# Performance work log

Measured on AMD Instinct MI355X. Metric: run time of the kernel, lower is better.

The kernel has to match this reference:

```python
import jax, jax.numpy as jnp
import numpy as np

DIM = 768
HEADS = 6
LEVELS = 3
POINTS = 4
HID = int(DIM * 0.25)  # 192
B = 4
H0 = 64
W0 = 64
NQ = H0 * W0
SHAPES = [(128, 128), (64, 64), (32, 32)]
NV = sum(h * w for h, w in SHAPES)
EPS = 1e-6


def _ln(x, g, b):
    m = x.mean(-1, keepdims=True)
    v = ((x - m) ** 2).mean(-1, keepdims=True)
    return (x - m) / jnp.sqrt(v + EPS) * g + b


def _bilinear(img, grid, Hl, Wl):
    # img: [BH, Hl*Wl, d], grid: [BH, Np, 2] in [-1,1] (x=width, y=height)
    # grid_sample semantics: bilinear, padding zeros, align_corners=False
    gx, gy = grid[..., 0], grid[..., 1]
    x = (gx + 1) * (Wl * 0.5) - 0.5
    y = (gy + 1) * (Hl * 0.5) - 0.5
    x0 = jnp.floor(x)
    y0 = jnp.floor(y)
    wx = x - x0
    wy = y - y0
    x0i = x0.astype(jnp.int32)
    y0i = y0.astype(jnp.int32)

    def corner(xi, yi, wgt):
        valid = (xi >= 0) & (xi < Wl) & (yi >= 0) & (yi < Hl)
        idx = jnp.clip(yi, 0, Hl - 1) * Wl + jnp.clip(xi, 0, Wl - 1)
        v = jnp.take_along_axis(img, idx[..., None], axis=1)
        return v * (wgt * valid)[..., None]

    return (corner(x0i, y0i, (1 - wx) * (1 - wy))
            + corner(x0i + 1, y0i, wx * (1 - wy))
            + corner(x0i, y0i + 1, (1 - wx) * wy)
            + corner(x0i + 1, y0i + 1, wx * wy))


def setup_inputs() -> dict:
    key = jax.random.key(0)
    ks = jax.random.split(key, 24)
    s = 0.02
    inp = {
        'query': jax.random.normal(ks[0], (B, NQ, DIM), jnp.float32),
        'reference_points': jax.random.uniform(ks[1], (B, NQ, LEVELS, 2), jnp.float32),
        'feat': jax.random.normal(ks[2], (B, NV, DIM), jnp.float32),
        'spatial_shapes': jnp.array(SHAPES, dtype=jnp.int32),
        'level_start_index': jnp.array(np.cumsum([0] + [h * w for h, w in SHAPES])[:-1], dtype=jnp.int32),
        'H': H0,
        'W': W0,
        'qn_g': jnp.ones((DIM,)), 'qn_b': jnp.zeros((DIM,)),
        'fn_g': jnp.ones((DIM,)), 'fn_b': jnp.zeros((DIM,)),
        'off_w': jax.random.normal(ks[3], (DIM, HEADS * LEVELS * POINTS * 2)) * s,
        'off_b': jax.random.normal(ks[4], (HEADS * LEVELS * POINTS * 2,)) * s,
        'aw_w': jax.random.normal(ks[5], (DIM, HEADS * LEVELS * POINTS)) * s,
        'aw_b': jnp.zeros((HEADS * LEVELS * POINTS,)),
        'vp_w': jax.random.normal(ks[6], (DIM, DIM)) * s,
        'vp_b': jnp.zeros((DIM,)),
        'op_w': jax.random.normal(ks[7], (DIM, DIM)) * s,
        'op_b': jnp.zeros((DIM,)),
        'ffn_g': jnp.ones((DIM,)), 'ffn_b': jnp.zeros((DIM,)),
        'fc1_w': jax.random.normal(ks[8], (DIM, HID)) * s,
        'fc1_b': jnp.zeros((HID,)),
        'dw_w': jax.random.normal(ks[9], (3, 3, 1, HID)) * s,
        'dw_b': jnp.zeros((HID,)),
        'fc2_w': jax.random.normal(ks[10], (HID, DIM)) * s,
        'fc2_b': jnp.zeros((DIM,)),
    }
    return inp


def reference(query, reference_points, feat, spatial_shapes, level_start_index, H, W,
              qn_g, qn_b, fn_g, fn_b, off_w, off_b, aw_w, aw_b, vp_w, vp_b, op_w, op_b,
              ffn_g, ffn_b, fc1_w, fc1_b, dw_w, dw_b, fc2_w, fc2_b):
    shapes = [(int(h), int(w)) for h, w in np.asarray(spatial_shapes)]
    starts = np.cumsum([0] + [h * w for h, w in shapes])[:-1]
    Bq, Nq, C = query.shape
    d = C // HEADS

    q = _ln(query, qn_g, qn_b)                       # query_norm
    v = _ln(feat, fn_g, fn_b) @ vp_w + vp_b          # feat_norm + value_proj
    v = v.reshape(Bq, -1, HEADS, d)

    off = (q @ off_w + off_b).reshape(Bq, Nq, HEADS, LEVELS, POINTS, 2)
    aw = (q @ aw_w + aw_b).reshape(Bq, Nq, HEADS, LEVELS * POINTS)
    aw = jax.nn.softmax(aw, axis=-1).reshape(Bq, Nq, HEADS, LEVELS, POINTS)

    # offset normalizer is (W, H) per level
    norm = jnp.array([[w_, h_] for h_, w_ in shapes], dtype=query.dtype)
    loc = reference_points[:, :, None, :, None, :] + off / norm[None, None, None, :, None, :]
    grids = 2.0 * loc - 1.0                          # [B,Nq,heads,L,P,2]

    outs = []
    for l, (hl, wl) in enumerate(shapes):
        vl = v[:, starts[l]:starts[l] + hl * wl]     # [B, hl*wl, heads, d]
        vl = vl.transpose(0, 2, 1, 3).reshape(Bq * HEADS, hl * wl, d)
        g = grids[:, :, :, l].transpose(0, 2, 1, 3, 4).reshape(Bq * HEADS, Nq * POINTS, 2)
        s = _bilinear(vl, g, hl, wl).reshape(Bq, HEADS, Nq, POINTS, d)
        outs.append(s)
    samp = jnp.stack(outs, axis=3)                   # [B,heads,Nq,L,P,d]
    w_att = aw.transpose(0, 2, 1, 3, 4)              # [B,heads,Nq,L,P]
    out = (samp * w_att[..., None]).sum(axis=(3, 4)) # [B,heads,Nq,d]
    out = out.transpose(0, 2, 1, 3).reshape(Bq, Nq, C)
    attn = out @ op_w + op_b + q                     # mmcv adds identity (=normed query)

    x = query + attn

    # ConvFFN: fc1 -> DWConv -> GELU -> fc2, residual
    y = _ln(x, ffn_g, ffn_b) @ fc1_w + fc1_b         # [B,Nq,HID]
    y2 = y.reshape(Bq, H, W, HID)
    y2 = jax.lax.conv_general_dilated(
        y2, dw_w, window_strides=(1, 1), padding='SAME',
        feature_group_count=HID,
        dimension_numbers=('NHWC', 'HWIO', 'NHWC')) + dw_b
    y = jax.nn.gelu(y2.reshape(Bq, Nq, HID), approximate=False)
    y = y @ fc2_w + fc2_b
    return x + y
```

## Files before the change

### kernel.cpp

```cpp
#include <hip/hip_runtime.h>
#include <hip/hip_bf16.h>

constexpr int kDIM = 768;
constexpr int kHEADS = 6;
constexpr int kLEVELS = 3;
constexpr int kPOINTS = 4;
constexpr int kHID = 192;
constexpr int kB = 4;
constexpr int kH0 = 64;
constexpr int kW0 = 64;
constexpr int kNQ = kH0 * kW0;
constexpr int kNV = 21504;
constexpr int kDH = 128;
constexpr float kEPS = 1e-6f;
constexpr int kOAW = 256;

typedef __attribute__((ext_vector_type(8))) short short8;
typedef __attribute__((ext_vector_type(4))) float floatx4;
typedef __attribute__((ext_vector_type(4))) unsigned int uintx4;

__device__ __forceinline__ float bf2f(__hip_bfloat16 x) { return __bfloat162float(x); }
__device__ __forceinline__ float bfu2f(unsigned short u) { return __uint_as_float(((unsigned)u) << 16); }
__device__ __forceinline__ unsigned short f2bfu(float f) {
  __hip_bfloat16 h = __float2bfloat16(f);
  return *reinterpret_cast<unsigned short*>(&h);
}

__global__ __launch_bounds__(256) void ln_bf16_kernel(
    const float* __restrict__ x, const float* __restrict__ g,
    const float* __restrict__ b, __hip_bfloat16* __restrict__ out)
{
  constexpr int MT = 8;
  int tid = threadIdx.x, grp = tid >> 5, lane = tid & 31;
  size_t row = (size_t)blockIdx.x * MT + grp;
  const float* xr = x + row * kDIM;
  float buf[kDIM / 32];
  float s = 0.f;
#pragma unroll
  for (int i = 0; i < kDIM / 32; ++i) { float v = xr[lane + i * 32]; buf[i] = v; s += v; }
  for (int d = 16; d > 0; d >>= 1) s += __shfl_down(s, d, 32);
  float mean = __shfl(s, 0, 32) * (1.f / kDIM);
  float vs = 0.f;
#pragma unroll
  for (int i = 0; i < kDIM / 32; ++i) { float d = buf[i] - mean; vs += d * d; }
  for (int d = 16; d > 0; d >>= 1) vs += __shfl_down(vs, d, 32);
  float rstd = rsqrtf(__shfl(vs, 0, 32) * (1.f / kDIM) + kEPS);
  __hip_bfloat16* orow = out + row * kDIM;
#pragma unroll
  for (int i = 0; i < kDIM / 32; ++i) {
    int k = lane + i * 32;
    orow[k] = __float2bfloat16((buf[i] - mean) * rstd * g[k] + b[k]);
  }
}

__global__ __launch_bounds__(256) void transpose_w_kernel(
    const float* __restrict__ w, __hip_bfloat16* __restrict__ wt)
{
  int t = blockIdx.x * 256 + threadIdx.x;
  int n = t / kDIM, k = t % kDIM;
  wt[t] = __float2bfloat16(w[(size_t)k * kDIM + n]);
}

template <int K, int N, int NPAD>
__global__ __launch_bounds__(256) void prep_wt_kernel(
    const float* __restrict__ w, const float* __restrict__ b,
    __hip_bfloat16* __restrict__ wt, float* __restrict__ bp)
{
  int t = blockIdx.x * 256 + threadIdx.x;
  int n = t / K, k = t % K;
  float v = (n < N) ? w[(size_t)k * N + n] : 0.f;
  wt[t] = __float2bfloat16(v);
  if (bp != nullptr && t < NPAD) bp[t] = (t < N) ? b[t] : 0.f;
}

__global__ __launch_bounds__(256) void prep_offaw_w_kernel(
    const float* __restrict__ ow, const float* __restrict__ aww,
    const float* __restrict__ ob, const float* __restrict__ awb,
    __hip_bfloat16* __restrict__ wt, float* __restrict__ bias)
{
  int t = blockIdx.x * 256 + threadIdx.x;
  int n = t / kDIM, k = t % kDIM;
  float v = 0.f;
  if (n < 144)       v = ow[(size_t)k * 144 + n];
  else if (n < 216)  v = aww[(size_t)k * 72 + (n - 144)];
  wt[t] = __float2bfloat16(v);
  if (t < kOAW) {
    float b = 0.f;
    if (t < 144)       b = ob[t];
    else if (t < 216)  b = awb[t - 144];
    bias[t] = b;
  }
}

template <int EPI, int KK>
__global__ __launch_bounds__(256) void gemm_bt_kernel(
    const unsigned short* __restrict__ A, const unsigned short* __restrict__ Bt,
    const float* __restrict__ bias,
    __hip_bfloat16* __restrict__ outB,
    const __hip_bfloat16* __restrict__ qln, const float* __restrict__ query,
    float* __restrict__ outF)
{
  constexpr int K = KK;
  constexpr int LDC = (EPI == 2) ? kOAW : kDIM;
  __shared__ unsigned short sA[128 * 64];
  __shared__ unsigned short sB[128 * 64];
  int tid = threadIdx.x;
  int wave = tid >> 6, lane = tid & 63;
  int tm = blockIdx.x * 128, tn = blockIdx.y * 128;
  int wm = (wave & 1) * 64, wn = (wave >> 1) * 64;
  floatx4 acc[4][4] = {};

  for (int k0 = 0; k0 < K; k0 += 64) {
    __syncthreads();
#pragma unroll
    for (int i = 0; i < 4; ++i) {
      int id = i * 256 + tid;
      int m = id >> 3, c = id & 7;
      uintx4 va = *(const uintx4*)(A + (size_t)(tm + m) * K + k0 + c * 8);
      *(uintx4*)((char*)sA + m * 128 + ((c ^ (m & 7)) * 16)) = va;
      uintx4 vb = *(const uintx4*)(Bt + (size_t)(tn + m) * K + k0 + c * 8);
      *(uintx4*)((char*)sB + m * 128 + ((c ^ (m & 7)) * 16)) = vb;
    }
    __syncthreads();
#pragma unroll
    for (int s = 0; s < 2; ++s) {
      int kc = s * 4 + (lane >> 4);
      short8 af[4], bfr[4];
#pragma unroll
      for (int i = 0; i < 4; ++i) {
        int mm = wm + i * 16 + (lane & 15);
        af[i] = *(const short8*)((const char*)sA + mm * 128 + ((kc ^ (mm & 7)) * 16));
        int nn = wn + i * 16 + (lane & 15);
        bfr[i] = *(const short8*)((const char*)sB + nn * 128 + ((kc ^ (nn & 7)) * 16));
      }
#pragma unroll
      for (int i = 0; i < 4; ++i)
#pragma unroll
        for (int j = 0; j < 4; ++j)
          acc[i][j] = __builtin_amdgcn_mfma_f32_16x16x32_bf16(af[i], bfr[j], acc[i][j], 0, 0, 0);
    }
  }

  int r0 = (lane >> 4) * 4, cc = lane & 15;
#pragma unroll
  for (int i = 0; i < 4; ++i) {
    int rowb = tm + wm + i * 16 + r0;
#pragma unroll
    for (int j = 0; j < 4; ++j) {
      int col = tn + wn + j * 16 + cc;
      float bv = bias[col];
#pragma unroll
      for (int r = 0; r < 4; ++r) {
        size_t o = (size_t)(rowb + r) * LDC + col;
        float val = acc[i][j][r] + bv;
        if constexpr (EPI == 0) {
          outB[o] = __float2bfloat16(val);
        } else if constexpr (EPI == 1) {
          outF[o] = val + bf2f(qln[o]) + query[o];
        } else if constexpr (EPI == 2) {
          outF[o] = val;
        } else {
          outF[o] = val + query[o];
        }
      }
    }
  }
}

__global__ __launch_bounds__(256) void aw_softmax_kernel(float* __restrict__ raw)
{
  int t = blockIdx.x * 256 + threadIdx.x;
  int row = t / kHEADS, h = t % kHEADS;
  float* p = raw + (size_t)row * kOAW + 144 + h * 12;
  float v[12];
  float m = -1e30f;
#pragma unroll
  for (int j = 0; j < 12; ++j) { v[j] = p[j]; m = fmaxf(m, v[j]); }
  float den = 0.f;
#pragma unroll
  for (int j = 0; j < 12; ++j) { v[j] = expf(v[j] - m); den += v[j]; }
  float inv = 1.f / den;
#pragma unroll
  for (int j = 0; j < 12; ++j) p[j] = v[j] * inv;
}

__global__ __launch_bounds__(192) void sample_kernel(
    const float* __restrict__ offaw,
    const float* __restrict__ refp, const __hip_bfloat16* __restrict__ v,
    __hip_bfloat16* __restrict__ samp)
{
  __shared__ int   idx_s[72][4];
  __shared__ float w_s[72][4];
  int bq = blockIdx.x;
  int b = bq >> 12;
  int tid = threadIdx.x;

  if (tid < 72) {
    const int LH[3] = {128, 64, 32};
    const int LST[3] = {0, 16384, 20480};
    int h2 = tid / 12, j = tid % 12, l = j >> 2, p = j & 3;
    int Wl = LH[l];
    const float* base = offaw + (size_t)bq * kOAW;
    float rx = refp[(size_t)bq * 6 + l * 2 + 0];
    float ry = refp[(size_t)bq * 6 + l * 2 + 1];
    float ox = base[h2 * 24 + l * 8 + p * 2 + 0];
    float oy = base[h2 * 24 + l * 8 + p * 2 + 1];
    float wgt = base[144 + h2 * 12 + l * 4 + p];
    float xx = rx * Wl + ox - 0.5f;
    float yy = ry * Wl + oy - 0.5f;
    float x0f = floorf(xx), y0f = floorf(yy);
    int x0 = (int)x0f, y0 = (int)y0f;
    float wx = xx - x0f, wy = yy - y0f;
#pragma unroll
    for (int cy = 0; cy < 2; ++cy) {
#pragma unroll
      for (int cx = 0; cx < 2; ++cx) {
        int xi = x0 + cx, yi = y0 + cy;
        bool valid = (xi >= 0) && (xi < Wl) && (yi >= 0) && (yi < Wl);
        int xc = min(max(xi, 0), Wl - 1), yc = min(max(yi, 0), Wl - 1);
        float cw = (cx ? wx : 1.f - wx) * (cy ? wy : 1.f - wy);
        idx_s[tid][cy * 2 + cx] = (LST[l] + yc * Wl + xc) * kDIM;
        w_s[tid][cy * 2 + cx] = valid ? cw * wgt : 0.f;
      }
    }
  }
  __syncthreads();

  int h = tid >> 5, c0 = (tid & 31) * 4;
  const __hip_bfloat16* vb = v + (size_t)b * kNV * kDIM + h * kDH + c0;
  float a0 = 0.f, a1 = 0.f, a2 = 0.f, a3 = 0.f;
#pragma unroll
  for (int j = 0; j < 12; ++j) {
    int t = h * 12 + j;
    int4 ii = *(const int4*)idx_s[t];
    float4 ww = *(const float4*)w_s[t];
#pragma unroll
    for (int k = 0; k < 4; ++k) {
      int idx = (k == 0) ? ii.x : (k == 1) ? ii.y : (k == 2) ? ii.z : ii.w;
      float wv = (k == 0) ? ww.x : (k == 1) ? ww.y : (k == 2) ? ww.z : ww.w;
      ushort4 uv = *(const ushort4*)(vb + idx);
      a0 += wv * bfu2f(uv.x);
      a1 += wv * bfu2f(uv.y);
      a2 += wv * bfu2f(uv.z);
      a3 += wv * bfu2f(uv.w);
    }
  }
  ushort4 ov;
  ov.x = f2bfu(a0); ov.y = f2bfu(a1); ov.z = f2bfu(a2); ov.w = f2bfu(a3);
  *(ushort4*)(samp + (size_t)bq * kDIM + h * kDH + c0) = ov;
}

__global__ __launch_bounds__(256) void dwconv_gelu_kernel(
    const float* __restrict__ y1, const float* __restrict__ w,
    const float* __restrict__ bias, __hip_bfloat16* __restrict__ y2)
{
  int idx = blockIdx.x * 256 + threadIdx.x;
  int c = idx % kHID;
  int sp = idx / kHID;
  int j = sp % kW0;
  int i = (sp / kW0) % kH0;
  int b = sp / (kW0 * kH0);
  float s = bias[c];
#pragma unroll
  for (int ky = 0; ky < 3; ++ky) {
    int yi = i + ky - 1;
    if (yi < 0 || yi >= kH0) continue;
#pragma unroll
    for (int kx = 0; kx < 3; ++kx) {
      int xj = j + kx - 1;
      if (xj < 0 || xj >= kW0) continue;
      s += y1[(((size_t)b * kH0 + yi) * kW0 + xj) * kOAW + c] * w[(ky * 3 + kx) * kHID + c];
    }
  }
  float gl = 0.5f * s * (1.f + erff(s * 0.70710678118654752440f));
  y2[idx] = __float2bfloat16(gl);
}

extern "C" void kernel_launch(void* const* d_in, const int* in_sizes, int n_in,
                              void* d_out, int out_size, void* d_ws, size_t ws_size,
                              hipStream_t stream)
{
  const float* query = (const float*)d_in[0];
  const float* refp  = (const float*)d_in[1];
  const float* feat  = (const float*)d_in[2];
  const float* qn_g  = (const float*)d_in[7];
  const float* qn_b  = (const float*)d_in[8];
  const float* fn_g  = (const float*)d_in[9];
  const float* fn_b  = (const float*)d_in[10];
  const float* off_w = (const float*)d_in[11];
  const float* off_b = (const float*)d_in[12];
  const float* aw_w  = (const float*)d_in[13];
  const float* aw_b  = (const float*)d_in[14];
  const float* vp_w  = (const float*)d_in[15];
  const float* vp_b  = (const float*)d_in[16];
  const float* op_w  = (const float*)d_in[17];
  const float* op_b  = (const float*)d_in[18];
  const float* ffn_g = (const float*)d_in[19];
  const float* ffn_b = (const float*)d_in[20];
  const float* fc1_w = (const float*)d_in[21];
  const float* fc1_b = (const float*)d_in[22];
  const float* dw_w  = (const float*)d_in[23];
  const float* dw_b  = (const float*)d_in[24];
  const float* fc2_w = (const float*)d_in[25];
  const float* fc2_b = (const float*)d_in[26];

  char* ws = (char*)d_ws;
  constexpr size_t kWsNeeded = 218400768ull;
  if (ws_size < kWsNeeded) return;

  __hip_bfloat16* a_ln     = (__hip_bfloat16*)(ws + 0);
  __hip_bfloat16* q_ln     = (__hip_bfloat16*)(ws + 0);
  __hip_bfloat16* x_ln     = (__hip_bfloat16*)(ws + 0);
  float*          y1p      = (float*)(ws + 25165824ull);
  __hip_bfloat16* samp     = (__hip_bfloat16*)(ws + 39321600ull);
  __hip_bfloat16* y2       = (__hip_bfloat16*)(ws + 41943040ull);
  __hip_bfloat16* v        = (__hip_bfloat16*)(ws + 66060288ull);
  float*          x        = (float*)(ws + 66060288ull);
  __hip_bfloat16* vp_w_t   = (__hip_bfloat16*)(ws + 198180864ull);
  __hip_bfloat16* op_w_t   = (__hip_bfloat16*)(ws + 199360512ull);
  float*          oa_raw   = (float*)(ws + 200540160ull);
  __hip_bfloat16* oa_wt    = (__hip_bfloat16*)(ws + 217317376ull);
  float*          oa_bias  = (float*)(ws + 217710592ull);
  __hip_bfloat16* fc1_wt   = (__hip_bfloat16*)(ws + 217711616ull);
  float*          fc1_bp   = (float*)(ws + 218104832ull);
  __hip_bfloat16* fc2_wt   = (__hip_bfloat16*)(ws + 218105856ull);

  constexpr int NROWQ = kB * kNQ;
  constexpr int NROWV = kB * kNV;
  constexpr int CHUNK = NROWV / 2;

  transpose_w_kernel<<<(kDIM * kDIM) / 256, 256, 0, stream>>>(vp_w, vp_w_t);
  transpose_w_kernel<<<(kDIM * kDIM) / 256, 256, 0, stream>>>(op_w, op_w_t);
  prep_offaw_w_kernel<<<(kOAW * kDIM) / 256, 256, 0, stream>>>(
      off_w, aw_w, off_b, aw_b, oa_wt, oa_bias);
  prep_wt_kernel<768, 192, 256><<<(256 * 768) / 256, 256, 0, stream>>>(
      fc1_w, fc1_b, fc1_wt, fc1_bp);
  prep_wt_kernel<192, 768, 768><<<(768 * 192) / 256, 256, 0, stream>>>(
      fc2_w, nullptr, fc2_wt, nullptr);

  for (int c = 0; c < 2; ++c) {
    ln_bf16_kernel<<<CHUNK / 8, 256, 0, stream>>>(
        feat + (size_t)c * CHUNK * kDIM, fn_g, fn_b, a_ln);
    gemm_bt_kernel<0, kDIM><<<dim3(CHUNK / 128, kDIM / 128), 256, 0, stream>>>(
        (const unsigned short*)a_ln, (const unsigned short*)vp_w_t, vp_b,
        v + (size_t)c * CHUNK * kDIM, nullptr, nullptr, nullptr);
  }

  ln_bf16_kernel<<<NROWQ / 8, 256, 0, stream>>>(query, qn_g, qn_b, q_ln);
  gemm_bt_kernel<2, kDIM><<<dim3(NROWQ / 128, kOAW / 128), 256, 0, stream>>>(
      (const unsigned short*)q_ln, (const unsigned short*)oa_wt, oa_bias,
      nullptr, nullptr, nullptr, oa_raw);
  aw_softmax_kernel<<<(NROWQ * kHEADS) / 256, 256, 0, stream>>>(oa_raw);
  sample_kernel<<<NROWQ, 192, 0, stream>>>(oa_raw, refp, v, samp);
  gemm_bt_kernel<1, kDIM><<<dim3(NROWQ / 128, kDIM / 128), 256, 0, stream>>>(
      (const unsigned short*)samp, (const unsigned short*)op_w_t, op_b,
      nullptr, q_ln, query, x);

  ln_bf16_kernel<<<NROWQ / 8, 256, 0, stream>>>(x, ffn_g, ffn_b, x_ln);
  gemm_bt_kernel<2, kDIM><<<dim3(NROWQ / 128, kOAW / 128), 256, 0, stream>>>(
      (const unsigned short*)x_ln, (const unsigned short*)fc1_wt, fc1_bp,
      nullptr, nullptr, nullptr, y1p);
  dwconv_gelu_kernel<<<(NROWQ * kHID) / 256, 256, 0, stream>>>(y1p, dw_w, dw_b, y2);
  gemm_bt_kernel<3, kHID><<<dim3(NROWQ / 128, kDIM / 128), 256, 0, stream>>>(
      (const unsigned short*)y2, (const unsigned short*)fc2_wt, fc2_b,
      nullptr, nullptr, x, (float*)d_out);
}
```

Measured before the change: 876.9 us.

## Use direct global-to-LDS loads in GEMM, swap grid order, widen sampler vectors

The GEMM tile loads now go straight from global memory into shared memory through the global_load_lds builtin. The XOR swizzle moves to the source address so the LDS layout stays the same, and the register round-trip is gone. The GEMM grid is transposed so consecutive blocks share the same A rows, which should help L2 reuse. The sampling kernel handles two queries per block with 8 channels per thread using 16-byte gathers, which halves the block count and widens each memory access. The direct-to-LDS path relies on the per-wave contiguous write pattern being correct.

```diff
diff --git a/kernel.cpp b/kernel.cpp
--- a/kernel.cpp
+++ b/kernel.cpp
@@ -20,11 +20,17 @@
 typedef __attribute__((ext_vector_type(4))) unsigned int uintx4;
 
 __device__ __forceinline__ float bf2f(__hip_bfloat16 x) { return __bfloat162float(x); }
-__device__ __forceinline__ float bfu2f(unsigned short u) { return __uint_as_float(((unsigned)u) << 16); }
+__device__ __forceinline__ float bflo2f(unsigned int u) { return __uint_as_float(u << 16); }
+__device__ __forceinline__ float bfhi2f(unsigned int u) { return __uint_as_float(u & 0xffff0000u); }
 __device__ __forceinline__ unsigned short f2bfu(float f) {
   __hip_bfloat16 h = __float2bfloat16(f);
   return *reinterpret_cast<unsigned short*>(&h);
 }
+
+#define GLD_LDS16(g, l) \
+  __builtin_amdgcn_global_load_lds( \
+      (const __attribute__((address_space(1))) void*)(g), \
+      (__attribute__((address_space(3))) void*)(l), 16, 0, 0)
 
 __global__ __launch_bounds__(256) void ln_bf16_kernel(
     const float* __restrict__ x, const float* __restrict__ g,
@@ -106,20 +112,24 @@
   __shared__ unsigned short sB[128 * 64];
   int tid = threadIdx.x;
   int wave = tid >> 6, lane = tid & 63;
-  int tm = blockIdx.x * 128, tn = blockIdx.y * 128;
+  int tm = blockIdx.y * 128, tn = blockIdx.x * 128;
   int wm = (wave & 1) * 64, wn = (wave >> 1) * 64;
   floatx4 acc[4][4] = {};
 
+  int sm_ = lane >> 3;
+  int sc_ = lane & 7;
+
   for (int k0 = 0; k0 < K; k0 += 64) {
     __syncthreads();
 #pragma unroll
     for (int i = 0; i < 4; ++i) {
-      int id = i * 256 + tid;
-      int m = id >> 3, c = id & 7;
-      uintx4 va = *(const uintx4*)(A + (size_t)(tm + m) * K + k0 + c * 8);
-      *(uintx4*)((char*)sA + m * 128 + ((c ^ (m & 7)) * 16)) = va;
-      uintx4 vb = *(const uintx4*)(Bt + (size_t)(tn + m) * K + k0 + c * 8);
-      *(uintx4*)((char*)sB + m * 128 + ((c ^ (m & 7)) * 16)) = vb;
+      int base_m = i * 32 + wave * 8;
+      int m = base_m + sm_;
+      int csrc = sc_ ^ (m & 7);
+      GLD_LDS16(A + (size_t)(tm + m) * K + k0 + csrc * 8,
+                (char*)sA + base_m * 128);
+      GLD_LDS16(Bt + (size_t)(tn + m) * K + k0 + csrc * 8,
+                (char*)sB + base_m * 128);
     }
     __syncthreads();
 #pragma unroll
@@ -189,16 +199,18 @@
     const float* __restrict__ refp, const __hip_bfloat16* __restrict__ v,
     __hip_bfloat16* __restrict__ samp)
 {
-  __shared__ int   idx_s[72][4];
-  __shared__ float w_s[72][4];
-  int bq = blockIdx.x;
-  int b = bq >> 12;
+  __shared__ __align__(16) int   idx_s[2][72][4];
+  __shared__ __align__(16) float w_s[2][72][4];
   int tid = threadIdx.x;
-
-  if (tid < 72) {
+  int bq0 = blockIdx.x * 2;
+
+  if (tid < 144) {
+    int q = (tid >= 72) ? 1 : 0;
+    int t = tid - q * 72;
+    int bq = bq0 + q;
     const int LH[3] = {128, 64, 32};
     const int LST[3] = {0, 16384, 20480};
-    int h2 = tid / 12, j = tid % 12, l = j >> 2, p = j & 3;
+    int h2 = t / 12, j = t % 12, l = j >> 2, p = j & 3;
     int Wl = LH[l];
     const float* base = offaw + (size_t)bq * kOAW;
     float rx = refp[(size_t)bq * 6 + l * 2 + 0];
@@ -219,35 +231,42 @@
         bool valid = (xi >= 0) && (xi < Wl) && (yi >= 0) && (yi < Wl);
         int xc = min(max(xi, 0), Wl - 1), yc = min(max(yi, 0), Wl - 1);
         float cw = (cx ? wx : 1.f - wx) * (cy ? wy : 1.f - wy);
-        idx_s[tid][cy * 2 + cx] = (LST[l] + yc * Wl + xc) * kDIM;
-        w_s[tid][cy * 2 + cx] = valid ? cw * wgt : 0.f;
+        idx_s[q][t][cy * 2 + cx] = (LST[l] + yc * Wl + xc) * kDIM;
+        w_s[q][t][cy * 2 + cx] = valid ? cw * wgt : 0.f;
       }
     }
   }
   __syncthreads();
 
-  int h = tid >> 5, c0 = (tid & 31) * 4;
+  int q = (tid >= 96) ? 1 : 0;
+  int t = tid - q * 96;
+  int bq = bq0 + q;
+  int b = bq >> 12;
+  int h = t >> 4, c0 = (t & 15) * 8;
   const __hip_bfloat16* vb = v + (size_t)b * kNV * kDIM + h * kDH + c0;
-  float a0 = 0.f, a1 = 0.f, a2 = 0.f, a3 = 0.f;
+  float a[8] = {};
 #pragma unroll
   for (int j = 0; j < 12; ++j) {
-    int t = h * 12 + j;
-    int4 ii = *(const int4*)idx_s[t];
-    float4 ww = *(const float4*)w_s[t];
+    int tt = h * 12 + j;
+    int4 ii = *(const int4*)idx_s[q][tt];
+    float4 ww = *(const float4*)w_s[q][tt];
 #pragma unroll
     for (int k = 0; k < 4; ++k) {
       int idx = (k == 0) ? ii.x : (k == 1) ? ii.y : (k == 2) ? ii.z : ii.w;
       float wv = (k == 0) ? ww.x : (k == 1) ? ww.y : (k == 2) ? ww.z : ww.w;
-      ushort4 uv = *(const ushort4*)(vb + idx);
-      a0 += wv * bfu2f(uv.x);
-      a1 += wv * bfu2f(uv.y);
-      a2 += wv * bfu2f(uv.z);
-      a3 += wv * bfu2f(uv.w);
-    }
-  }
-  ushort4 ov;
-  ov.x = f2bfu(a0); ov.y = f2bfu(a1); ov.z = f2bfu(a2); ov.w = f2bfu(a3);
-  *(ushort4*)(samp + (size_t)bq * kDIM + h * kDH + c0) = ov;
+      uintx4 uv = *(const uintx4*)(vb + idx);
+      a[0] += wv * bflo2f(uv.x); a[1] += wv * bfhi2f(uv.x);
+      a[2] += wv * bflo2f(uv.y); a[3] += wv * bfhi2f(uv.y);
+      a[4] += wv * bflo2f(uv.z); a[5] += wv * bfhi2f(uv.z);
+      a[6] += wv * bflo2f(uv.w); a[7] += wv * bfhi2f(uv.w);
+    }
+  }
+  uintx4 ov;
+  ov.x = (unsigned)f2bfu(a[0]) | ((unsigned)f2bfu(a[1]) << 16);
+  ov.y = (unsigned)f2bfu(a[2]) | ((unsigned)f2bfu(a[3]) << 16);
+  ov.z = (unsigned)f2bfu(a[4]) | ((unsigned)f2bfu(a[5]) << 16);
+  ov.w = (unsigned)f2bfu(a[6]) | ((unsigned)f2bfu(a[7]) << 16);
+  *(uintx4*)(samp + (size_t)bq * kDIM + h * kDH + c0) = ov;
 }
 
 __global__ __launch_bounds__(256) void dwconv_gelu_kernel(
@@ -341,27 +360,27 @@
   for (int c = 0; c < 2; ++c) {
     ln_bf16_kernel<<<CHUNK / 8, 256, 0, stream>>>(
         feat + (size_t)c * CHUNK * kDIM, fn_g, fn_b, a_ln);
-    gemm_bt_kernel<0, kDIM><<<dim3(CHUNK / 128, kDIM / 128), 256, 0, stream>>>(
+    gemm_bt_kernel<0, kDIM><<<dim3(kDIM / 128, CHUNK / 128), 256, 0, stream>>>(
         (const unsigned short*)a_ln, (const unsigned short*)vp_w_t, vp_b,
         v + (size_t)c * CHUNK * kDIM, nullptr, nullptr, nullptr);
   }
 
   ln_bf16_kernel<<<NROWQ / 8, 256, 0, stream>>>(query, qn_g, qn_b, q_ln);
-  gemm_bt_kernel<2, kDIM><<<dim3(NROWQ / 128, kOAW / 128), 256, 0, stream>>>(
+  gemm_bt_kernel<2, kDIM><<<dim3(kOAW / 128, NROWQ / 128), 256, 0, stream>>>(
       (const unsigned short*)q_ln, (const unsigned short*)oa_wt, oa_bias,
       nullptr, nullptr, nullptr, oa_raw);
   aw_softmax_kernel<<<(NROWQ * kHEADS) / 256, 256, 0, stream>>>(oa_raw);
-  sample_kernel<<<NROWQ, 192, 0, stream>>>(oa_raw, refp, v, samp);
-  gemm_bt_kernel<1, kDIM><<<dim3(NROWQ / 128, kDIM / 128), 256, 0, stream>>>(
+  sample_kernel<<<NROWQ / 2, 192, 0, stream>>>(oa_raw, refp, v, samp);
+  gemm_bt_kernel<1, kDIM><<<dim3(kDIM / 128, NROWQ / 128), 256, 0, stream>>>(
       (const unsigned short*)samp, (const unsigned short*)op_w_t, op_b,
       nullptr, q_ln, query, x);
 
   ln_bf16_kernel<<<NROWQ / 8, 256, 0, stream>>>(x, ffn_g, ffn_b, x_ln);
-  gemm_bt_kernel<2, kDIM><<<dim3(NROWQ / 128, kOAW / 128), 256, 0, stream>>>(
+  gemm_bt_kernel<2, kDIM><<<dim3(kOAW / 128, NROWQ / 128), 256, 0, stream>>>(
       (const unsigned short*)x_ln, (const unsigned short*)fc1_wt, fc1_bp,
       nullptr, nullptr, nullptr, y1p);
   dwconv_gelu_kernel<<<(NROWQ * kHID) / 256, 256, 0, stream>>>(y1p, dw_w, dw_b, y2);
-  gemm_bt_kernel<3, kHID><<<dim3(NROWQ / 128, kDIM / 128), 256, 0, stream>>>(
+  gemm_bt_kernel<3, kHID><<<dim3(kDIM / 128, NROWQ / 128), 256, 0, stream>>>(
       (const unsigned short*)y2, (const unsigned short*)fc2_wt, fc2_b,
       nullptr, nullptr, x, (float*)d_out);
 }
```

Result: no change. 869.7 us (-0.8%).
